# Kernel tuning notes

Hardware: AMD Instinct MI355X
Metric: run time of the kernel (lower is better)

The kernel has to match this reference:

```python
import jax, jax.numpy as jnp
import numpy as np

B, CIN, COUT, H, W = 8, 128, 256, 64, 64
EPS = 1e-5


def conv2d(x, w, b, pad):
    y = jax.lax.conv_general_dilated(
        x, w, window_strides=(1, 1), padding=[(pad, pad), (pad, pad)],
        dimension_numbers=('NCHW', 'OIHW', 'NCHW'))
    return y + b[None, :, None, None]


def deform_sample(x, offset):
    # x: [B,C,H,W], offset: [B,18,H,W] -> sampled: [B,C,9,H,W]
    b, c, h, w = x.shape
    off = offset.reshape(b, 9, 2, h, w)  # (dy, dx) per kernel tap (torchvision v1 order)
    ky = (jnp.arange(9) // 3 - 1).astype(x.dtype)
    kx = (jnp.arange(9) % 3 - 1).astype(x.dtype)
    py = jnp.arange(h, dtype=x.dtype)[None, None, :, None] + ky[None, :, None, None] + off[:, :, 0]
    px = jnp.arange(w, dtype=x.dtype)[None, None, None, :] + kx[None, :, None, None] + off[:, :, 1]
    y0 = jnp.floor(py); x0 = jnp.floor(px)
    fy = py - y0;       fx = px - x0
    xf = x.reshape(b, c, h * w)

    def gather(iy, ix):
        valid = (iy >= 0) & (iy < h) & (ix >= 0) & (ix < w)
        iyc = jnp.clip(iy, 0, h - 1).astype(jnp.int32)
        ixc = jnp.clip(ix, 0, w - 1).astype(jnp.int32)
        idx = (iyc * w + ixc).reshape(b, -1)  # [B, 9*H*W]
        g = jax.vmap(lambda xb, ib: jnp.take(xb, ib, axis=1))(xf, idx)  # [B,C,9HW]
        return g.reshape(b, c, 9, h, w) * valid.astype(x.dtype)[:, None]

    samp = (gather(y0,     x0    ) * ((1 - fy) * (1 - fx))[:, None]
          + gather(y0,     x0 + 1) * ((1 - fy) * fx      )[:, None]
          + gather(y0 + 1, x0    ) * (fy * (1 - fx)      )[:, None]
          + gather(y0 + 1, x0 + 1) * (fy * fx            )[:, None])
    return samp


def setup_inputs():
    key = jax.random.key(0)
    ks = jax.random.split(key, 8)
    return {
        'x':     jax.random.normal(ks[0], (B, CIN, H, W), jnp.float32),
        'w_off': jax.random.normal(ks[1], (18, CIN, 3, 3), jnp.float32) * 0.01,
        'b_off': jnp.zeros((18,), jnp.float32),
        'w_def': jax.random.normal(ks[2], (COUT, CIN, 3, 3), jnp.float32) * 0.03,
        'b_def': jax.random.normal(ks[3], (COUT,), jnp.float32) * 0.01,
        'gamma': jnp.ones((COUT,), jnp.float32),
        'beta':  jnp.zeros((COUT,), jnp.float32),
        'w_sc':  jax.random.normal(ks[4], (COUT, CIN, 1, 1), jnp.float32) * 0.05,
        'b_sc':  jnp.zeros((COUT,), jnp.float32),
    }


def reference(x, w_off, b_off, w_def, b_def, gamma, beta, w_sc, b_sc):
    offset = conv2d(x, w_off, b_off, pad=1)                 # [B,18,H,W]
    samp = deform_sample(x, offset)                         # [B,C,9,H,W]
    out = jnp.einsum('bckhw,ock->bohw', samp, w_def.reshape(COUT, CIN, 9))
    out = out + b_def[None, :, None, None]
    # BatchNorm2d (training mode: batch statistics)
    mean = out.mean(axis=(0, 2, 3))
    var = out.var(axis=(0, 2, 3))
    out = (out - mean[None, :, None, None]) * jax.lax.rsqrt(var + EPS)[None, :, None, None]
    out = out * gamma[None, :, None, None] + beta[None, :, None, None]
    out = out + conv2d(x, w_sc, b_sc, pad=0)                # residual shortcut (1x1)
    return jax.nn.relu(out)
```

## Files before the change

kernel.cpp:

```cpp
#include <hip/hip_runtime.h>

typedef __attribute__((ext_vector_type(8))) short bf16x8;
typedef __attribute__((ext_vector_type(4))) float f32x4;

__device__ __forceinline__ float bf2f(unsigned short u) {
  return __uint_as_float(((unsigned int)u) << 16);
}
__device__ __forceinline__ unsigned short f2bf(float f) {
  unsigned int u = __float_as_uint(f);
  u += 0x7fffu + ((u >> 16) & 1u);
  return (unsigned short)(u >> 16);
}

constexpr size_t OFF_XPAD = 0;
constexpr size_t SZ_XPAD  = (size_t)8 * 66 * 66 * 128 * 2;
constexpr size_t OFF_WB   = OFF_XPAD + SZ_XPAD;
constexpr size_t SZ_WB    = (size_t)9 * 16 * 256 * 8 * 2;
constexpr size_t OFF_WS2  = OFF_WB + SZ_WB;
constexpr size_t SZ_WS2   = (size_t)16 * 256 * 8 * 2;
constexpr size_t OFF_WO   = OFF_WS2 + SZ_WS2;
constexpr size_t SZ_WO    = (size_t)9 * 16 * 32 * 8 * 2;
constexpr size_t OFF_YM   = OFF_WO + SZ_WO;
constexpr size_t SZ_YM    = (size_t)256 * 32768 * 2;
constexpr size_t OFF_PART = OFF_YM + SZ_YM;
constexpr size_t SZ_PART  = (size_t)1024 * 256 * 2 * 4;
constexpr size_t OFF_STAT = OFF_PART + SZ_PART;

__global__ __launch_bounds__(256) void k_prep_x(const float* __restrict__ x,
                                                unsigned short* __restrict__ xp) {
  int blk = blockIdx.x;
  int b = blk >> 7, h = (blk >> 1) & 63, chalf = blk & 1;
  int t = threadIdx.x;
  __shared__ float tile[16][66];
  for (int cc = 0; cc < 4; ++cc) {
    int c0 = (chalf * 4 + cc) * 16;
    int wr = t & 63, cl = t >> 6;
#pragma unroll
    for (int i = 0; i < 4; ++i) {
      int c = c0 + cl * 4 + i;
      tile[cl * 4 + i][wr] = x[(((size_t)b * 128 + c) * 64 + h) * 64 + wr];
    }
    __syncthreads();
    int ww = t >> 2, cq = t & 3;
    ushort4 u4;
    u4.x = f2bf(tile[cq * 4 + 0][ww]);
    u4.y = f2bf(tile[cq * 4 + 1][ww]);
    u4.z = f2bf(tile[cq * 4 + 2][ww]);
    u4.w = f2bf(tile[cq * 4 + 3][ww]);
    *(ushort4*)(xp + ((size_t)(b * 66 + h + 1) * 66 + (ww + 1)) * 128 + c0 + cq * 4) = u4;
    __syncthreads();
  }
}

__global__ __launch_bounds__(256) void k_pack_w(const float* __restrict__ wdef,
                                                const float* __restrict__ wsc,
                                                const float* __restrict__ woff,
                                                unsigned short* __restrict__ wB,
                                                unsigned short* __restrict__ wS,
                                                unsigned short* __restrict__ wO) {
  int tid = blockIdx.x * 256 + threadIdx.x;
  if (tid < 294912) {
    int k8 = tid & 7, n = (tid >> 3) & 255, kb = (tid >> 11) & 15, tap = tid >> 15;
    int c = kb * 8 + k8;
    wB[tid] = f2bf(wdef[((size_t)n * 128 + c) * 9 + tap]);
  } else if (tid < 294912 + 32768) {
    int i = tid - 294912;
    int k8 = i & 7, n = (i >> 3) & 255, kb = i >> 11;
    wS[i] = f2bf(wsc[(size_t)n * 128 + kb * 8 + k8]);
  } else if (tid < 294912 + 32768 + 36864) {
    int i = tid - 327680;
    int k8 = i & 7, n = (i >> 3) & 31, kb = (i >> 8) & 15, tap = i >> 12;
    int c = kb * 8 + k8;
    wO[i] = f2bf(n < 18 ? woff[((size_t)n * 128 + c) * 9 + tap] : 0.f);
  }
}

__global__ __launch_bounds__(256, 4) void k_main(const unsigned short* __restrict__ xp,
                                                 const unsigned short* __restrict__ wB,
                                                 const unsigned short* __restrict__ wO,
                                                 const float* __restrict__ boff,
                                                 const float* __restrict__ bdef,
                                                 unsigned short* __restrict__ ymain,
                                                 float* __restrict__ partials) {
  int blk = blockIdx.x;
  int b = blk >> 7, h = (blk >> 1) & 63, half = blk & 1;
  int px0 = half * 32;
  int t = threadIdx.x;
  int lane = t & 63, wid = t >> 6;
  int m = lane & 15, quad = lane >> 4;
  __shared__ __align__(16) unsigned short At[2][32 * 136];
  __shared__ float offsL[9][32][2];

  if (wid < 2) {
    f32x4 a0 = {0.f, 0.f, 0.f, 0.f}, a1 = {0.f, 0.f, 0.f, 0.f};
    int px = wid * 16 + m;
    const unsigned short* xbase = xp + ((size_t)(b * 66 + h) * 66 + px0 + px) * 128 + quad * 8;
    for (int tap = 0; tap < 9; ++tap) {
      const unsigned short* arow = xbase + ((tap / 3) * 66 + (tap % 3)) * 128;
#pragma unroll
      for (int kk = 0; kk < 4; ++kk) {
        bf16x8 a = *(const bf16x8*)(arow + kk * 32);
        const unsigned short* bb = wO + (size_t)(tap * 16 + kk * 4 + quad) * 256;
        bf16x8 b0 = *(const bf16x8*)(bb + m * 8);
        bf16x8 b1 = *(const bf16x8*)(bb + (16 + m) * 8);
        a0 = __builtin_amdgcn_mfma_f32_16x16x32_bf16(a, b0, a0, 0, 0, 0);
        a1 = __builtin_amdgcn_mfma_f32_16x16x32_bf16(a, b1, a1, 0, 0, 0);
      }
    }
#pragma unroll
    for (int r = 0; r < 4; ++r) {
      int pxs = wid * 16 + quad * 4 + r;
      offsL[m >> 1][pxs][m & 1] = a0[r] + boff[m];
      if (m < 2) offsL[8][pxs][m] = a1[r] + boff[16 + m];
    }
  }
  __syncthreads();

  f32x4 acc[2][4];
#pragma unroll
  for (int i = 0; i < 2; ++i)
#pragma unroll
    for (int j = 0; j < 4; ++j) acc[i][j] = (f32x4){0.f, 0.f, 0.f, 0.f};

  int px_s = t >> 3, sub = t & 7;
  const unsigned short* xb_base = xp + (size_t)b * 66 * 66 * 128;
  int nb = wid * 64;

  auto sample_prep = [&](int tap, float* wgt, const unsigned short** p) {
    float2 ov = *(const float2*)&offsL[tap][px_s][0];
    int ky = tap / 3 - 1, kx = tap % 3 - 1;
    float py = (float)(h + ky) + ov.x;
    float pxf = (float)(px0 + px_s + kx) + ov.y;
    float y0f = floorf(py), x0f = floorf(pxf);
    float fy = py - y0f, fx = pxf - x0f;
    int iy0 = (int)y0f, ix0 = (int)x0f;
#pragma unroll
    for (int j = 0; j < 4; ++j) {
      int iy = iy0 + (j >> 1), ix = ix0 + (j & 1);
      float wy = (j >> 1) ? fy : 1.f - fy;
      float wx = (j & 1) ? fx : 1.f - fx;
      bool valid = (iy >= 0) && (iy < 64) && (ix >= 0) && (ix < 64);
      int iyc = min(max(iy, 0), 63), ixc = min(max(ix, 0), 63);
      wgt[j] = valid ? wy * wx : 0.f;
      p[j] = xb_base + ((size_t)(iyc + 1) * 66 + (ixc + 1)) * 128 + sub * 8;
    }
  };
  auto load_all = [&](const unsigned short** p, bf16x8 (*v)[4]) {
#pragma unroll
    for (int g = 0; g < 2; ++g)
#pragma unroll
      for (int j = 0; j < 4; ++j)
        v[g][j] = *(const bf16x8*)(p[j] + g * 64);
  };
  auto store_all = [&](unsigned short* dst, const float* wgt, bf16x8 (*v)[4]) {
#pragma unroll
    for (int g = 0; g < 2; ++g) {
      bf16x8 o;
#pragma unroll
      for (int j = 0; j < 8; ++j) {
        float s = fmaf(wgt[0], bf2f((unsigned short)v[g][0][j]),
                  fmaf(wgt[1], bf2f((unsigned short)v[g][1][j]),
                  fmaf(wgt[2], bf2f((unsigned short)v[g][2][j]),
                       wgt[3] * bf2f((unsigned short)v[g][3][j]))));
        o[j] = (short)f2bf(s);
      }
      *(bf16x8*)(dst + g * 64) = o;
    }
  };
  auto mfma_tap = [&](const unsigned short* buf, int tap) {
#pragma unroll
    for (int kk = 0; kk < 4; ++kk) {
      bf16x8 af[2];
#pragma unroll
      for (int ms = 0; ms < 2; ++ms)
        af[ms] = *(const bf16x8*)(buf + (ms * 16 + m) * 136 + kk * 32 + quad * 8);
#pragma unroll
      for (int ns = 0; ns < 4; ++ns) {
        bf16x8 bfr = *(const bf16x8*)(wB + ((size_t)(tap * 16 + kk * 4 + quad) * 256 + nb + ns * 16 + m) * 8);
#pragma unroll
        for (int ms = 0; ms < 2; ++ms)
          acc[ms][ns] = __builtin_amdgcn_mfma_f32_16x16x32_bf16(af[ms], bfr, acc[ms][ns], 0, 0, 0);
      }
    }
  };

  {
    float wgt[4]; const unsigned short* p[4]; bf16x8 v[2][4];
    sample_prep(0, wgt, p);
    load_all(p, v);
    store_all(&At[0][px_s * 136 + sub * 8], wgt, v);
  }
#pragma unroll
  for (int tap = 0; tap < 9; ++tap) {
    __syncthreads();
    const unsigned short* cur = At[tap & 1];
    if (tap < 8) {
      float wgt[4]; const unsigned short* p[4]; bf16x8 v[2][4];
      sample_prep(tap + 1, wgt, p);
      load_all(p, v);
      mfma_tap(cur, tap);
      store_all(&At[(tap + 1) & 1][px_s * 136 + sub * 8], wgt, v);
    } else {
      mfma_tap(cur, tap);
    }
  }

  __syncthreads();
  unsigned short* yb = &At[0][0];
#pragma unroll
  for (int ns = 0; ns < 4; ++ns) {
    int n = nb + ns * 16 + m;
    float bias = bdef[n];
    float s = 0.f, q = 0.f;
#pragma unroll
    for (int ms = 0; ms < 2; ++ms) {
#pragma unroll
      for (int r = 0; r < 4; ++r) {
        int px = ms * 16 + quad * 4 + r;
        float v = acc[ms][ns][r] + bias;
        yb[px * 258 + n] = f2bf(v);
        s += v;
        q += v * v;
      }
    }
    s += __shfl_xor(s, 16); s += __shfl_xor(s, 32);
    q += __shfl_xor(q, 16); q += __shfl_xor(q, 32);
    if (quad == 0) {
      partials[((size_t)blk * 256 + n) * 2 + 0] = s;
      partials[((size_t)blk * 256 + n) * 2 + 1] = q;
    }
  }
  __syncthreads();
  {
    int px_l = t & 31, n_g = t >> 5;
    const unsigned short* col = yb + px_l * 258;
    unsigned short* gdst = ymain + blk * 32 + px_l;
#pragma unroll
    for (int i = 0; i < 32; ++i) {
      int n = n_g * 32 + i;
      gdst[(size_t)n * 32768] = col[n];
    }
  }
}

__global__ __launch_bounds__(64) void k_stats(const float* __restrict__ partials,
                                              const float* __restrict__ gamma,
                                              const float* __restrict__ beta,
                                              float* __restrict__ stats) {
  int ch = blockIdx.x;
  int L = threadIdx.x;
  float s = 0.f, q = 0.f;
#pragma unroll
  for (int i = 0; i < 16; ++i) {
    int row = i * 64 + L;
    s += partials[((size_t)row * 256 + ch) * 2 + 0];
    q += partials[((size_t)row * 256 + ch) * 2 + 1];
  }
#pragma unroll
  for (int d = 1; d < 64; d <<= 1) { s += __shfl_xor(s, d); q += __shfl_xor(q, d); }
  if (L == 0) {
    float mean = s * (1.f / 32768.f);
    float var = q * (1.f / 32768.f) - mean * mean;
    float inv = rsqrtf(var + 1e-5f);
    float A = gamma[ch] * inv;
    stats[ch * 2 + 0] = A;
    stats[ch * 2 + 1] = beta[ch] - mean * A;
  }
}

__global__ __launch_bounds__(256, 4) void k_final(const unsigned short* __restrict__ xp,
                                                  const unsigned short* __restrict__ wS,
                                                  const unsigned short* __restrict__ ymain,
                                                  const float* __restrict__ stats,
                                                  const float* __restrict__ bsc,
                                                  float* __restrict__ out) {
  int blk = blockIdx.x;
  int b = blk >> 7, h = (blk >> 1) & 63, half = blk & 1;
  int t = threadIdx.x;
  int lane = t & 63, wid = t >> 6;
  int m = lane & 15, quad = lane >> 4;
  f32x4 acc[4][2];
#pragma unroll
  for (int i = 0; i < 4; ++i)
#pragma unroll
    for (int j = 0; j < 2; ++j) acc[i][j] = (f32x4){0.f, 0.f, 0.f, 0.f};
  const unsigned short* xrow = xp + ((size_t)(b * 66 + h + 1) * 66 + 1 + half * 32) * 128;
  int nb = wid * 64;
#pragma unroll
  for (int kk = 0; kk < 4; ++kk) {
    bf16x8 xf[2];
#pragma unroll
    for (int pt = 0; pt < 2; ++pt)
      xf[pt] = *(const bf16x8*)(xrow + (pt * 16 + m) * 128 + kk * 32 + quad * 8);
#pragma unroll
    for (int ct = 0; ct < 4; ++ct) {
      bf16x8 wf = *(const bf16x8*)(wS + ((size_t)(kk * 4 + quad) * 256 + nb + ct * 16 + m) * 8);
#pragma unroll
      for (int pt = 0; pt < 2; ++pt)
        acc[ct][pt] = __builtin_amdgcn_mfma_f32_16x16x32_bf16(wf, xf[pt], acc[ct][pt], 0, 0, 0);
    }
  }
#pragma unroll
  for (int ct = 0; ct < 4; ++ct) {
#pragma unroll
    for (int r = 0; r < 4; ++r) {
      int ch = nb + ct * 16 + quad * 4 + r;
      float A = stats[ch * 2], Bc = stats[ch * 2 + 1];
      float bs = bsc[ch] + Bc;
#pragma unroll
      for (int pt = 0; pt < 2; ++pt) {
        int px = pt * 16 + m;
        float ym = bf2f(ymain[(size_t)ch * 32768 + blk * 32 + px]);
        float v = fmaxf(fmaf(ym, A, bs) + acc[ct][pt][r], 0.f);
        out[(((size_t)(b * 256 + ch) * 64 + h) * 64) + half * 32 + px] = v;
      }
    }
  }
}

extern "C" void kernel_launch(void* const* d_in, const int* in_sizes, int n_in,
                              void* d_out, int out_size, void* d_ws, size_t ws_size,
                              hipStream_t stream) {
  const float* x     = (const float*)d_in[0];
  const float* w_off = (const float*)d_in[1];
  const float* b_off = (const float*)d_in[2];
  const float* w_def = (const float*)d_in[3];
  const float* b_def = (const float*)d_in[4];
  const float* gamma = (const float*)d_in[5];
  const float* beta  = (const float*)d_in[6];
  const float* w_sc  = (const float*)d_in[7];
  const float* b_sc  = (const float*)d_in[8];
  float* out = (float*)d_out;

  char* ws = (char*)d_ws;
  unsigned short* xpad  = (unsigned short*)(ws + OFF_XPAD);
  unsigned short* wB    = (unsigned short*)(ws + OFF_WB);
  unsigned short* wS    = (unsigned short*)(ws + OFF_WS2);
  unsigned short* wO    = (unsigned short*)(ws + OFF_WO);
  unsigned short* ymain = (unsigned short*)(ws + OFF_YM);
  float* partials       = (float*)(ws + OFF_PART);
  float* stats          = (float*)(ws + OFF_STAT);

  hipMemsetAsync(xpad, 0, SZ_XPAD, stream);
  k_prep_x<<<1024, 256, 0, stream>>>(x, xpad);
  k_pack_w<<<1424, 256, 0, stream>>>(w_def, w_sc, w_off, wB, wS, wO);
  k_main<<<1024, 256, 0, stream>>>(xpad, wB, wO, b_off, b_def, ymain, partials);
  k_stats<<<256, 64, 0, stream>>>(partials, gamma, beta, stats);
  k_final<<<1024, 256, 0, stream>>>(xpad, wS, ymain, stats, b_sc, out);
}
```

Measured before the change: 165.1 us.

## Merge prep kernels, replace stats pass with atomics, split final kernel over channels

Fuses the x-padding and weight-packing kernels into one launch. BN partial sums are now accumulated with float atomics in k_main, which removes the separate k_stats kernel; k_final computes mean and variance inline per channel. k_final's grid is doubled by splitting output channels into halves, giving more blocks with fewer accumulators each. Launch-bounds occupancy hints are dropped and bf16 packing uses the paired conversion intrinsic. Atomics add contention (1024 blocks × 256 channels) and make the sums depend on summation order.

```diff
diff --git a/kernel.cpp b/kernel.cpp
--- a/kernel.cpp
+++ b/kernel.cpp
@@ -1,4 +1,5 @@
 #include <hip/hip_runtime.h>
+#include <hip/hip_bf16.h>
 
 typedef __attribute__((ext_vector_type(8))) short bf16x8;
 typedef __attribute__((ext_vector_type(4))) float f32x4;
@@ -10,6 +11,10 @@
   unsigned int u = __float_as_uint(f);
   u += 0x7fffu + ((u >> 16) & 1u);
   return (unsigned short)(u >> 16);
+}
+__device__ __forceinline__ int f2bf2(float lo, float hi) {
+  __hip_bfloat162 h = __float22bfloat162_rn(float2{lo, hi});
+  return *(int*)&h;
 }
 
 constexpr size_t OFF_XPAD = 0;
@@ -22,66 +27,66 @@
 constexpr size_t SZ_WO    = (size_t)9 * 16 * 32 * 8 * 2;
 constexpr size_t OFF_YM   = OFF_WO + SZ_WO;
 constexpr size_t SZ_YM    = (size_t)256 * 32768 * 2;
-constexpr size_t OFF_PART = OFF_YM + SZ_YM;
-constexpr size_t SZ_PART  = (size_t)1024 * 256 * 2 * 4;
-constexpr size_t OFF_STAT = OFF_PART + SZ_PART;
-
-__global__ __launch_bounds__(256) void k_prep_x(const float* __restrict__ x,
-                                                unsigned short* __restrict__ xp) {
+constexpr size_t OFF_SUMS = OFF_YM + SZ_YM;
+constexpr size_t SZ_SUMS  = (size_t)256 * 2 * 4;
+
+__global__ __launch_bounds__(256) void k_prep(const float* __restrict__ x,
+                                              const float* __restrict__ wdef,
+                                              const float* __restrict__ wsc,
+                                              const float* __restrict__ woff,
+                                              unsigned short* __restrict__ xp,
+                                              unsigned short* __restrict__ wB,
+                                              unsigned short* __restrict__ wS,
+                                              unsigned short* __restrict__ wO) {
   int blk = blockIdx.x;
-  int b = blk >> 7, h = (blk >> 1) & 63, chalf = blk & 1;
   int t = threadIdx.x;
-  __shared__ float tile[16][66];
-  for (int cc = 0; cc < 4; ++cc) {
-    int c0 = (chalf * 4 + cc) * 16;
-    int wr = t & 63, cl = t >> 6;
-#pragma unroll
-    for (int i = 0; i < 4; ++i) {
-      int c = c0 + cl * 4 + i;
-      tile[cl * 4 + i][wr] = x[(((size_t)b * 128 + c) * 64 + h) * 64 + wr];
-    }
-    __syncthreads();
-    int ww = t >> 2, cq = t & 3;
-    ushort4 u4;
-    u4.x = f2bf(tile[cq * 4 + 0][ww]);
-    u4.y = f2bf(tile[cq * 4 + 1][ww]);
-    u4.z = f2bf(tile[cq * 4 + 2][ww]);
-    u4.w = f2bf(tile[cq * 4 + 3][ww]);
-    *(ushort4*)(xp + ((size_t)(b * 66 + h + 1) * 66 + (ww + 1)) * 128 + c0 + cq * 4) = u4;
-    __syncthreads();
-  }
-}
-
-__global__ __launch_bounds__(256) void k_pack_w(const float* __restrict__ wdef,
-                                                const float* __restrict__ wsc,
-                                                const float* __restrict__ woff,
-                                                unsigned short* __restrict__ wB,
-                                                unsigned short* __restrict__ wS,
-                                                unsigned short* __restrict__ wO) {
-  int tid = blockIdx.x * 256 + threadIdx.x;
-  if (tid < 294912) {
-    int k8 = tid & 7, n = (tid >> 3) & 255, kb = (tid >> 11) & 15, tap = tid >> 15;
-    int c = kb * 8 + k8;
-    wB[tid] = f2bf(wdef[((size_t)n * 128 + c) * 9 + tap]);
-  } else if (tid < 294912 + 32768) {
-    int i = tid - 294912;
-    int k8 = i & 7, n = (i >> 3) & 255, kb = i >> 11;
-    wS[i] = f2bf(wsc[(size_t)n * 128 + kb * 8 + k8]);
-  } else if (tid < 294912 + 32768 + 36864) {
-    int i = tid - 327680;
-    int k8 = i & 7, n = (i >> 3) & 31, kb = (i >> 8) & 15, tap = i >> 12;
-    int c = kb * 8 + k8;
-    wO[i] = f2bf(n < 18 ? woff[((size_t)n * 128 + c) * 9 + tap] : 0.f);
-  }
-}
-
-__global__ __launch_bounds__(256, 4) void k_main(const unsigned short* __restrict__ xp,
-                                                 const unsigned short* __restrict__ wB,
-                                                 const unsigned short* __restrict__ wO,
-                                                 const float* __restrict__ boff,
-                                                 const float* __restrict__ bdef,
-                                                 unsigned short* __restrict__ ymain,
-                                                 float* __restrict__ partials) {
+  if (blk < 1024) {
+    int b = blk >> 7, h = (blk >> 1) & 63, chalf = blk & 1;
+    __shared__ float tile[16][66];
+    for (int cc = 0; cc < 4; ++cc) {
+      int c0 = (chalf * 4 + cc) * 16;
+      int wr = t & 63, cl = t >> 6;
+#pragma unroll
+      for (int i = 0; i < 4; ++i) {
+        int c = c0 + cl * 4 + i;
+        tile[cl * 4 + i][wr] = x[(((size_t)b * 128 + c) * 64 + h) * 64 + wr];
+      }
+      __syncthreads();
+      int ww = t >> 2, cq = t & 3;
+      ushort4 u4;
+      u4.x = f2bf(tile[cq * 4 + 0][ww]);
+      u4.y = f2bf(tile[cq * 4 + 1][ww]);
+      u4.z = f2bf(tile[cq * 4 + 2][ww]);
+      u4.w = f2bf(tile[cq * 4 + 3][ww]);
+      *(ushort4*)(xp + ((size_t)(b * 66 + h + 1) * 66 + (ww + 1)) * 128 + c0 + cq * 4) = u4;
+      __syncthreads();
+    }
+  } else {
+    int tid = (blk - 1024) * 256 + t;
+    if (tid < 294912) {
+      int k8 = tid & 7, n = (tid >> 3) & 255, kb = (tid >> 11) & 15, tap = tid >> 15;
+      int c = kb * 8 + k8;
+      wB[tid] = f2bf(wdef[((size_t)n * 128 + c) * 9 + tap]);
+    } else if (tid < 294912 + 32768) {
+      int i = tid - 294912;
+      int k8 = i & 7, n = (i >> 3) & 255, kb = i >> 11;
+      wS[i] = f2bf(wsc[(size_t)n * 128 + kb * 8 + k8]);
+    } else if (tid < 294912 + 32768 + 36864) {
+      int i = tid - 327680;
+      int k8 = i & 7, n = (i >> 3) & 31, kb = (i >> 8) & 15, tap = i >> 12;
+      int c = kb * 8 + k8;
+      wO[i] = f2bf(n < 18 ? woff[((size_t)n * 128 + c) * 9 + tap] : 0.f);
+    }
+  }
+}
+
+__global__ __launch_bounds__(256) void k_main(const unsigned short* __restrict__ xp,
+                                              const unsigned short* __restrict__ wB,
+                                              const unsigned short* __restrict__ wO,
+                                              const float* __restrict__ boff,
+                                              const float* __restrict__ bdef,
+                                              unsigned short* __restrict__ ymain,
+                                              float* __restrict__ sums) {
   int blk = blockIdx.x;
   int b = blk >> 7, h = (blk >> 1) & 63, half = blk & 1;
   int px0 = half * 32;
@@ -155,16 +160,19 @@
   auto store_all = [&](unsigned short* dst, const float* wgt, bf16x8 (*v)[4]) {
 #pragma unroll
     for (int g = 0; g < 2; ++g) {
-      bf16x8 o;
-#pragma unroll
-      for (int j = 0; j < 8; ++j) {
-        float s = fmaf(wgt[0], bf2f((unsigned short)v[g][0][j]),
-                  fmaf(wgt[1], bf2f((unsigned short)v[g][1][j]),
-                  fmaf(wgt[2], bf2f((unsigned short)v[g][2][j]),
-                       wgt[3] * bf2f((unsigned short)v[g][3][j]))));
-        o[j] = (short)f2bf(s);
-      }
-      *(bf16x8*)(dst + g * 64) = o;
+      float s[8];
+#pragma unroll
+      for (int j = 0; j < 8; ++j)
+        s[j] = fmaf(wgt[0], bf2f((unsigned short)v[g][0][j]),
+               fmaf(wgt[1], bf2f((unsigned short)v[g][1][j]),
+               fmaf(wgt[2], bf2f((unsigned short)v[g][2][j]),
+                    wgt[3] * bf2f((unsigned short)v[g][3][j]))));
+      int4 o;
+      o.x = f2bf2(s[0], s[1]);
+      o.y = f2bf2(s[2], s[3]);
+      o.z = f2bf2(s[4], s[5]);
+      o.w = f2bf2(s[6], s[7]);
+      *(int4*)(dst + g * 64) = o;
     }
   };
   auto mfma_tap = [&](const unsigned short* buf, int tap) {
@@ -226,8 +234,8 @@
     s += __shfl_xor(s, 16); s += __shfl_xor(s, 32);
     q += __shfl_xor(q, 16); q += __shfl_xor(q, 32);
     if (quad == 0) {
-      partials[((size_t)blk * 256 + n) * 2 + 0] = s;
-      partials[((size_t)blk * 256 + n) * 2 + 1] = q;
+      atomicAdd(&sums[n * 2 + 0], s);
+      atomicAdd(&sums[n * 2 + 1], q);
     }
   }
   __syncthreads();
@@ -243,49 +251,27 @@
   }
 }
 
-__global__ __launch_bounds__(64) void k_stats(const float* __restrict__ partials,
-                                              const float* __restrict__ gamma,
-                                              const float* __restrict__ beta,
-                                              float* __restrict__ stats) {
-  int ch = blockIdx.x;
-  int L = threadIdx.x;
-  float s = 0.f, q = 0.f;
-#pragma unroll
-  for (int i = 0; i < 16; ++i) {
-    int row = i * 64 + L;
-    s += partials[((size_t)row * 256 + ch) * 2 + 0];
-    q += partials[((size_t)row * 256 + ch) * 2 + 1];
-  }
-#pragma unroll
-  for (int d = 1; d < 64; d <<= 1) { s += __shfl_xor(s, d); q += __shfl_xor(q, d); }
-  if (L == 0) {
-    float mean = s * (1.f / 32768.f);
-    float var = q * (1.f / 32768.f) - mean * mean;
-    float inv = rsqrtf(var + 1e-5f);
-    float A = gamma[ch] * inv;
-    stats[ch * 2 + 0] = A;
-    stats[ch * 2 + 1] = beta[ch] - mean * A;
-  }
-}
-
-__global__ __launch_bounds__(256, 4) void k_final(const unsigned short* __restrict__ xp,
-                                                  const unsigned short* __restrict__ wS,
-                                                  const unsigned short* __restrict__ ymain,
-                                                  const float* __restrict__ stats,
-                                                  const float* __restrict__ bsc,
-                                                  float* __restrict__ out) {
+__global__ __launch_bounds__(256) void k_final(const unsigned short* __restrict__ xp,
+                                               const unsigned short* __restrict__ wS,
+                                               const unsigned short* __restrict__ ymain,
+                                               const float* __restrict__ sums,
+                                               const float* __restrict__ gamma,
+                                               const float* __restrict__ beta,
+                                               const float* __restrict__ bsc,
+                                               float* __restrict__ out) {
   int blk = blockIdx.x;
-  int b = blk >> 7, h = (blk >> 1) & 63, half = blk & 1;
+  int chalf = blk & 1, half = (blk >> 1) & 1, h = (blk >> 2) & 63, b = blk >> 8;
+  int rowblk = blk >> 1;
   int t = threadIdx.x;
   int lane = t & 63, wid = t >> 6;
   int m = lane & 15, quad = lane >> 4;
-  f32x4 acc[4][2];
-#pragma unroll
-  for (int i = 0; i < 4; ++i)
+  f32x4 acc[2][2];
+#pragma unroll
+  for (int i = 0; i < 2; ++i)
 #pragma unroll
     for (int j = 0; j < 2; ++j) acc[i][j] = (f32x4){0.f, 0.f, 0.f, 0.f};
   const unsigned short* xrow = xp + ((size_t)(b * 66 + h + 1) * 66 + 1 + half * 32) * 128;
-  int nb = wid * 64;
+  int nb = chalf * 128 + wid * 32;
 #pragma unroll
   for (int kk = 0; kk < 4; ++kk) {
     bf16x8 xf[2];
@@ -293,7 +279,7 @@
     for (int pt = 0; pt < 2; ++pt)
       xf[pt] = *(const bf16x8*)(xrow + (pt * 16 + m) * 128 + kk * 32 + quad * 8);
 #pragma unroll
-    for (int ct = 0; ct < 4; ++ct) {
+    for (int ct = 0; ct < 2; ++ct) {
       bf16x8 wf = *(const bf16x8*)(wS + ((size_t)(kk * 4 + quad) * 256 + nb + ct * 16 + m) * 8);
 #pragma unroll
       for (int pt = 0; pt < 2; ++pt)
@@ -301,17 +287,20 @@
     }
   }
 #pragma unroll
-  for (int ct = 0; ct < 4; ++ct) {
+  for (int ct = 0; ct < 2; ++ct) {
 #pragma unroll
     for (int r = 0; r < 4; ++r) {
       int ch = nb + ct * 16 + quad * 4 + r;
-      float A = stats[ch * 2], Bc = stats[ch * 2 + 1];
-      float bs = bsc[ch] + Bc;
+      float s = sums[ch * 2], q = sums[ch * 2 + 1];
+      float mean = s * (1.f / 32768.f);
+      float var = q * (1.f / 32768.f) - mean * mean;
+      float A = gamma[ch] * rsqrtf(var + 1e-5f);
+      float Bc = beta[ch] - mean * A + bsc[ch];
 #pragma unroll
       for (int pt = 0; pt < 2; ++pt) {
         int px = pt * 16 + m;
-        float ym = bf2f(ymain[(size_t)ch * 32768 + blk * 32 + px]);
-        float v = fmaxf(fmaf(ym, A, bs) + acc[ct][pt][r], 0.f);
+        float ym = bf2f(ymain[(size_t)ch * 32768 + rowblk * 32 + px]);
+        float v = fmaxf(fmaf(ym, A, Bc) + acc[ct][pt][r], 0.f);
         out[(((size_t)(b * 256 + ch) * 64 + h) * 64) + half * 32 + px] = v;
       }
     }
@@ -338,13 +327,11 @@
   unsigned short* wS    = (unsigned short*)(ws + OFF_WS2);
   unsigned short* wO    = (unsigned short*)(ws + OFF_WO);
   unsigned short* ymain = (unsigned short*)(ws + OFF_YM);
-  float* partials       = (float*)(ws + OFF_PART);
-  float* stats          = (float*)(ws + OFF_STAT);
+  float* sums           = (float*)(ws + OFF_SUMS);
 
   hipMemsetAsync(xpad, 0, SZ_XPAD, stream);
-  k_prep_x<<<1024, 256, 0, stream>>>(x, xpad);
-  k_pack_w<<<1424, 256, 0, stream>>>(w_def, w_sc, w_off, wB, wS, wO);
-  k_main<<<1024, 256, 0, stream>>>(xpad, wB, wO, b_off, b_def, ymain, partials);
-  k_stats<<<256, 64, 0, stream>>>(partials, gamma, beta, stats);
-  k_final<<<1024, 256, 0, stream>>>(xpad, wS, ymain, stats, b_sc, out);
-}
+  hipMemsetAsync(sums, 0, SZ_SUMS, stream);
+  k_prep<<<2448, 256, 0, stream>>>(x, w_def, w_sc, w_off, xpad, wB, wS, wO);
+  k_main<<<1024, 256, 0, stream>>>(xpad, wB, wO, b_off, b_def, ymain, sums);
+  k_final<<<2048, 256, 0, stream>>>(xpad, wS, ymain, sums, gamma, beta, b_sc, out);
+}
```

Measured after the change: 223.9 us. 1.36x slower.
